# Performance work log

Measured on AMD Instinct MI355X. Metric: run time of the kernel, lower is better.

Reference implementation:

```python
import jax, jax.numpy as jnp
import numpy as np

MAX_LAB = 64  # cap on connected-component ids per sample (original cc3d is unbounded)
BIG = jnp.int32(2 ** 30)


def _cc_label(mask):
    """26-connectivity connected components of a 3D bool mask via label propagation.
    Each component ends with label == max initial voxel id in it (nonzero), bg = 0."""
    n = mask.size
    init = jnp.where(mask, jnp.arange(1, n + 1, dtype=jnp.int32).reshape(mask.shape), jnp.int32(0))

    def cond(st):
        return jnp.any(st[0] != st[1])

    def body(st):
        lab = st[0]
        # max over 3x3x3 neighborhood == 26-connectivity propagation step
        neigh = jax.lax.reduce_window(lab, jnp.int32(0), jax.lax.max, (3, 3, 3), (1, 1, 1), 'SAME')
        return (jnp.where(mask, neigh, jnp.int32(0)), lab)

    lab, _ = jax.lax.while_loop(cond, body, (init, jnp.full_like(init, -1)))
    return lab


def _compact(lab):
    """Relabel a per-sample label map to consecutive ids 0,1..k (0 = background),
    matching cc3d's 1..k numbering."""
    u = jnp.unique(lab, size=MAX_LAB + 1, fill_value=BIG)  # sorted: [0, l1, .., lk, BIG..]
    return jnp.searchsorted(u, lab).astype(jnp.int32)


def _instance_dice(x, y):
    xb = jnp.squeeze(x, 1) > 0.5  # [B,D,H,W] pred foreground
    yb = jnp.squeeze(y, 1) > 0.5  # [B,D,H,W] gt foreground
    label = jax.vmap(lambda m: _compact(_cc_label(m)))
    gt_lab = label(yb)  # per-sample ids 0..k_i (ids shared across batch, as in original)
    pr_lab = label(xb)
    M = MAX_LAB + 1
    # joint histogram over (gt component id, pred component id), global across batch
    idx = gt_lab.reshape(-1) * M + pr_lab.reshape(-1)
    overlap = jax.ops.segment_sum(jnp.ones(idx.shape, jnp.float32), idx, num_segments=M * M).reshape(M, M)
    gt_size = overlap.sum(1)  # [M] voxels per gt id
    pr_size = overlap.sum(0)  # [M] voxels per pred id
    ov = overlap[1:, 1:]                       # [G,P] fg-fg overlaps
    inter_mask = ov > 0                        # pred comp p intersects gt comp g
    inter = ov.sum(1)                          # [G] |gt_g  ∩  union(intersecting preds)|
    union_sz = (inter_mask * pr_size[1:]).sum(1)  # [G] |union of intersecting pred comps|
    has_inter = inter > 0
    dice = jnp.where(has_inter, 2.0 * inter / jnp.maximum(union_sz + gt_size[1:], 1.0), 0.0)
    lesion_dice = dice.sum()
    num_gt = jnp.sum(gt_size[1:] > 0).astype(jnp.float32)
    tp_mask = inter_mask.any(0)                # [P] pred comps matched to some gt
    num_fp = jnp.sum((pr_size[1:] > 0) & ~tp_mask).astype(jnp.float32)
    return lesion_dice / (num_gt + num_fp)


def setup_inputs() -> dict:
    B, D, H, W = 2, 128, 128, 128
    R, N_BLOBS = 5, 12
    rng = np.random.default_rng(0)
    zz, yy, xx = np.meshgrid(np.arange(D), np.arange(H), np.arange(W), indexing='ij')

    def blobs(k):
        m = np.zeros((B, D, H, W), bool)
        for b in range(B):
            c = rng.integers(R + 2, D - R - 2, size=(k, 3))
            for cz, cy, cx in c:
                m[b] |= (zz - cz) ** 2 + (yy - cy) ** 2 + (xx - cx) ** 2 <= R * R
        return m

    y = blobs(N_BLOBS)
    # prediction = slightly shifted gt (partial-overlap TPs) + extra false-positive blobs
    x = np.roll(y, shift=(2, 1, 0), axis=(1, 2, 3)) | blobs(4)
    return {"x": jnp.asarray(x[:, None].astype(np.float32)),
            "y": jnp.asarray(y[:, None].astype(np.float32))}


def reference(x, y):
    return _instance_dice(x, y)
```

## Files before the change

### kernel.cpp

```cpp
#include <hip/hip_runtime.h>


#define NVOX (128 * 128 * 128)
#define NTOT (2 * NVOX)
#define NBLK 4096
#define CAP 12288
#define ML 65
#define NSLAB 8
#define ZSLAB 16

__global__ __launch_bounds__(256) void k_count(
    const float4* __restrict__ x, const float4* __restrict__ y,
    unsigned char* __restrict__ maskArr, int* __restrict__ blkCnt) {
    int t = blockIdx.x * 256 + threadIdx.x;
    float4 xv = x[t];
    float4 yv = y[t];
    unsigned m = 0;
    if (xv.x > 0.5f) m |= 1u;
    if (xv.y > 0.5f) m |= 2u;
    if (xv.z > 0.5f) m |= 4u;
    if (xv.w > 0.5f) m |= 8u;
    if (yv.x > 0.5f) m |= 16u;
    if (yv.y > 0.5f) m |= 32u;
    if (yv.z > 0.5f) m |= 64u;
    if (yv.w > 0.5f) m |= 128u;
    maskArr[t] = (unsigned char)m;
    int pk = __popc(m & 0xFu) | (__popc(m >> 4) << 16);
    __shared__ int red[256];
    red[threadIdx.x] = pk;
    __syncthreads();
    for (int s = 128; s > 0; s >>= 1) {
        if ((int)threadIdx.x < s) red[threadIdx.x] += red[threadIdx.x + s];
        __syncthreads();
    }
    if (threadIdx.x == 0) {
        blkCnt[blockIdx.x]        = red[0] & 0xFFFF;
        blkCnt[NBLK + blockIdx.x] = red[0] >> 16;
    }
}

__global__ __launch_bounds__(1024) void k_scan(
    const int* __restrict__ blkCnt, int* __restrict__ blkOff, int* __restrict__ cnt) {
    __shared__ int buf[2][1024];
    __shared__ int segbase;
    int t = threadIdx.x;
    for (int f = 0; f < 2; ++f) {
        const int* c = blkCnt + f * NBLK;
        int* o = blkOff + f * NBLK;
        int base = t * 4;
        int a0 = c[base], a1 = c[base + 1], a2 = c[base + 2], a3 = c[base + 3];
        int s = a0 + a1 + a2 + a3;
        int src = 0;
        buf[0][t] = s;
        __syncthreads();
        for (int d = 1; d < 1024; d <<= 1) {
            int nv = buf[src][t];
            if (t >= d) nv += buf[src][t - d];
            buf[src ^ 1][t] = nv;
            src ^= 1;
            __syncthreads();
        }
        int incl = buf[src][t];
        int excl = incl - s;
        if (t == 511) segbase = incl;
        __syncthreads();
        int sub = (base >= 2048) ? segbase : 0;
        o[base]     = excl - sub;
        o[base + 1] = excl + a0 - sub;
        o[base + 2] = excl + a0 + a1 - sub;
        o[base + 3] = excl + a0 + a1 + a2 - sub;
        if (t == 511)  cnt[f * 2 + 0] = incl;
        if (t == 1023) cnt[f * 2 + 1] = incl - segbase;
        __syncthreads();
    }
}

__global__ __launch_bounds__(256) void k_fill(
    const unsigned char* __restrict__ maskArr, const int* __restrict__ blkOff,
    unsigned short* __restrict__ posMapX, unsigned short* __restrict__ posMapY,
    int* __restrict__ lists) {
    int blk = blockIdx.x;
    int t = blk * 256 + threadIdx.x;
    int b = blk >> 11;
    unsigned m = maskArr[t];
    int px = __popc(m & 0xFu), py = __popc(m >> 4);
    __shared__ int buf[2][256];
    int pk = px | (py << 16);
    int src = 0;
    buf[0][threadIdx.x] = pk;
    __syncthreads();
    for (int d = 1; d < 256; d <<= 1) {
        int nv = buf[src][threadIdx.x];
        if ((int)threadIdx.x >= d) nv += buf[src][threadIdx.x - d];
        buf[src ^ 1][threadIdx.x] = nv;
        src ^= 1;
        __syncthreads();
    }
    int incl = buf[src][threadIdx.x];
    int baseX = blkOff[blk]        + (incl & 0xFFFF) - px;
    int baseY = blkOff[NBLK + blk] + (incl >> 16)    - py;
    int i = t << 2;
    int j = i & (NVOX - 1);
    ushort4 pxv, pyv;
    unsigned short* ppx = &pxv.x;
    unsigned short* ppy = &pyv.x;
    int cx = 0, cy = 0;
    #pragma unroll
    for (int k = 0; k < 4; ++k) {
        unsigned short vx = 0, vy = 0;
        if (m & (1u << k)) {
            int pos = baseX + cx++;
            if (pos < CAP) { lists[(0 + b) * CAP + pos] = j + k; vx = (unsigned short)(pos + 1); }
        }
        if (m & (1u << (k + 4))) {
            int pos = baseY + cy++;
            if (pos < CAP) { lists[(2 + b) * CAP + pos] = j + k; vy = (unsigned short)(pos + 1); }
        }
        ppx[k] = vx;
        ppy[k] = vy;
    }
    ((ushort4*)posMapX)[t] = pxv;
    ((ushort4*)posMapY)[t] = pyv;
}

__device__ __forceinline__ int find_root(volatile unsigned* parent, int i) {
    unsigned p = parent[i];
    while (p != (unsigned)i) {
        unsigned gp = parent[p];
        if (gp != p) parent[i] = gp;
        i = (int)p;
        p = gp;
    }
    return i;
}

__device__ __forceinline__ void lds_union(unsigned* parentNV, int a, int b) {
    volatile unsigned* parent = (volatile unsigned*)parentNV;
    int ra = find_root(parent, a);
    int rb = find_root(parent, b);
    while (ra != rb) {
        int lo = ra < rb ? ra : rb;
        int hi = ra < rb ? rb : ra;
        unsigned old = atomicCAS(&parentNV[lo], (unsigned)lo, (unsigned)hi);
        if (old == (unsigned)lo) return;
        ra = find_root(parent, (int)old);
        rb = find_root(parent, hi);
    }
}

__global__ __launch_bounds__(1024) void k_cc_local(
    const unsigned short* __restrict__ posMapX, const unsigned short* __restrict__ posMapY,
    const int* __restrict__ lists, const int* __restrict__ blkOff,
    const int* __restrict__ cnt, int* __restrict__ rootPos) {
    int fb = blockIdx.y;
    int slab = blockIdx.x;
    int f = fb >> 1, b = fb & 1;
    const unsigned short* posMap = (f ? posMapY : posMapX) + (b << 21);
    const int* fgl = lists + fb * CAP;
    int n = cnt[fb]; if (n > CAP) n = CAP;
    int blkbase = b * 2048 + slab * 256;
    int s0 = blkOff[f * NBLK + blkbase];
    int s1 = (slab == NSLAB - 1) ? n : blkOff[f * NBLK + blkbase + 256];
    if (s1 > n) s1 = n;
    int ns = s1 - s0;
    if (ns <= 0) return;

    __shared__ unsigned parent[CAP];
    int tid = threadIdx.x;

    for (int q = tid; q < ns; q += 1024) {
        int p = s0 + q;
        int j = fgl[p];
        unsigned par = (unsigned)q;
        if (p + 1 < s1 && (j & 127) != 127) {
            if (fgl[p + 1] == j + 1) par = (unsigned)(q + 1);
        }
        parent[q] = par;
    }
    __syncthreads();

    for (int q = tid; q < ns; q += 1024) {
        int j = fgl[s0 + q];
        int z = j >> 14, y = (j >> 7) & 127, x0 = j & 127;
        bool ztop = ((z & (ZSLAB - 1)) == (ZSLAB - 1));
        unsigned short qv[12];
        int idx = 0;
        #pragma unroll
        for (int dx = -1; dx <= 1; ++dx) {
            int yy = y + 1, xx = x0 + dx;
            bool ok = yy <= 127 && (unsigned)xx <= 127u;
            int nj = (z << 14) + (yy << 7) + xx;
            qv[idx++] = ok ? posMap[nj] : (unsigned short)0;
        }
        #pragma unroll
        for (int dy = -1; dy <= 1; ++dy)
            #pragma unroll
            for (int dx = -1; dx <= 1; ++dx) {
                int zz = z + 1, yy = y + dy, xx = x0 + dx;
                bool ok = !ztop && zz <= 127 && (unsigned)yy <= 127u && (unsigned)xx <= 127u;
                int nj = (zz << 14) + (yy << 7) + xx;
                qv[idx++] = ok ? posMap[nj] : (unsigned short)0;
            }
        #pragma unroll
        for (int k = 0; k < 12; ++k)
            if (qv[k]) lds_union(parent, q, (int)qv[k] - 1 - s0);
    }
    __syncthreads();

    for (int q = tid; q < ns; q += 1024)
        rootPos[fb * CAP + s0 + q] = s0 + find_root((volatile unsigned*)parent, q);
}

__global__ __launch_bounds__(1024) void k_cc_merge(
    const unsigned short* __restrict__ posMapX, const unsigned short* __restrict__ posMapY,
    const int* __restrict__ lists, const int* __restrict__ cnt,
    const int* __restrict__ rootPos, unsigned char* __restrict__ compact) {
    int fb = blockIdx.x;
    int f = fb >> 1, b = fb & 1;
    const unsigned short* posMap = (f ? posMapY : posMapX) + (b << 21);
    const int* fgl = lists + fb * CAP;
    unsigned char* cmp = compact + fb * CAP;
    int tid = threadIdx.x;
    int n = cnt[fb]; if (n > CAP) n = CAP;

    __shared__ unsigned parent[CAP];
    __shared__ int rootsL[128];
    __shared__ int sortedL[64];
    __shared__ int nrSh;

    for (int p = tid; p < n; p += 1024) parent[p] = (unsigned)rootPos[fb * CAP + p];
    if (tid == 0) nrSh = 0;
    __syncthreads();

    for (int p = tid; p < n; p += 1024) {
        int j = fgl[p];
        int z = j >> 14;
        if ((z & (ZSLAB - 1)) != (ZSLAB - 1) || z == 127) continue;
        int y = (j >> 7) & 127, x0 = j & 127;
        int zz = z + 1;
        unsigned short qv[9];
        int idx = 0;
        #pragma unroll
        for (int dy = -1; dy <= 1; ++dy)
            #pragma unroll
            for (int dx = -1; dx <= 1; ++dx) {
                int yy = y + dy, xx = x0 + dx;
                bool ok = (unsigned)yy <= 127u && (unsigned)xx <= 127u;
                int nj = (zz << 14) + (yy << 7) + xx;
                qv[idx++] = ok ? posMap[nj] : (unsigned short)0;
            }
        #pragma unroll
        for (int k = 0; k < 9; ++k)
            if (qv[k]) lds_union(parent, p, (int)qv[k] - 1);
    }
    __syncthreads();

    for (int p = tid; p < n; p += 1024) {
        if (parent[p] == (unsigned)p) {
            int slot = atomicAdd(&nrSh, 1);
            if (slot < 128) rootsL[slot] = p;
        }
    }
    __syncthreads();
    int nr = nrSh; if (nr > 64) nr = 64;
    if (tid < nr) {
        int v = rootsL[tid];
        int r = 0;
        for (int k = 0; k < nr; ++k) r += (rootsL[k] < v) ? 1 : 0;
        sortedL[r] = v;
    }
    __syncthreads();

    for (int p = tid; p < n; p += 1024) {
        int r = find_root((volatile unsigned*)parent, p);
        int lo = 0, hi = nr;
        while (lo < hi) { int mid = (lo + hi) >> 1; if (sortedL[mid] < r) lo = mid + 1; else hi = mid; }
        cmp[p] = (unsigned char)(lo + 1);
    }
}

__global__ __launch_bounds__(256) void k_overlap(
    const unsigned short* __restrict__ posMapX, const unsigned short* __restrict__ posMapY,
    const int* __restrict__ lists, const int* __restrict__ cnt,
    const unsigned char* __restrict__ compact, int* __restrict__ overlap) {
    int fb = blockIdx.y;
    int f = fb >> 1, b = fb & 1;
    int n = cnt[fb]; if (n > CAP) n = CAP;
    int t = blockIdx.x * blockDim.x + threadIdx.x;
    if (t >= n) return;
    int j = lists[fb * CAP + t];
    int gi = (b << 21) + j;
    int key;
    if (f == 0) {
        int pc = (int)compact[fb * CAP + t];
        int q = (int)posMapY[gi];
        int gc = q ? (int)compact[(2 + b) * CAP + (q - 1)] : 0;
        key = gc * ML + pc;
    } else {
        if (posMapX[gi] != 0) return;
        int gc = (int)compact[fb * CAP + t];
        key = gc * ML;
    }
    unsigned long long remaining = __ballot(1);
    int lane = threadIdx.x & 63;
    while (remaining) {
        int leader = __ffsll(remaining) - 1;
        int lkey = __shfl(key, leader);
        unsigned long long m = __ballot(lkey == key ? 1 : 0) & remaining;
        if (lane == leader) atomicAdd(&overlap[lkey], (int)__popcll(m));
        remaining &= ~m;
    }
}

__global__ void k_final(const int* __restrict__ overlap, float* __restrict__ out) {
    __shared__ int O[ML * ML];
    __shared__ float prs[ML];
    __shared__ unsigned char tp[ML];
    __shared__ float diceSh[ML];
    __shared__ int ngSh[ML];
    __shared__ int nfSh[ML];
    int tid = threadIdx.x;
    for (int i = tid; i < ML * ML; i += blockDim.x) O[i] = overlap[i];
    __syncthreads();
    if (tid < ML) {
        int s = 0; int any = 0;
        for (int g = 0; g < ML; ++g) {
            int o = O[g * ML + tid];
            s += o;
            if (g >= 1 && o > 0) any = 1;
        }
        prs[tid] = (float)s;
        tp[tid] = (unsigned char)any;
    }
    __syncthreads();
    if (tid < ML) {
        float dice = 0.f; int ng = 0, nf = 0;
        if (tid >= 1) {
            int gt = 0, inter = 0; float un = 0.f;
            for (int p = 0; p < ML; ++p) {
                int o = O[tid * ML + p];
                gt += o;
                if (p >= 1) { inter += o; if (o > 0) un += prs[p]; }
            }
            if (inter > 0) {
                float den = un + (float)gt;
                if (den < 1.f) den = 1.f;
                dice = 2.f * (float)inter / den;
            }
            ng = (gt > 0) ? 1 : 0;
            nf = (prs[tid] > 0.f && tp[tid] == 0) ? 1 : 0;
        }
        diceSh[tid] = dice; ngSh[tid] = ng; nfSh[tid] = nf;
    }
    __syncthreads();
    if (tid == 0) {
        float ld = 0.f; int ng = 0, nf = 0;
        for (int k = 1; k < ML; ++k) { ld += diceSh[k]; ng += ngSh[k]; nf += nfSh[k]; }
        out[0] = ld / (float)(ng + nf);
    }
}

extern "C" void kernel_launch(void* const* d_in, const int* in_sizes, int n_in,
                              void* d_out, int out_size, void* d_ws, size_t ws_size,
                              hipStream_t stream) {
    const float* x = (const float*)d_in[0];
    const float* y = (const float*)d_in[1];
    float* out = (float*)d_out;

    char* base = (char*)d_ws;
    int* cnt            = (int*)base;
    int* overlap        = cnt + 16;
    int* blkCnt         = overlap + ML * ML;
    int* blkOff         = blkCnt + 2 * NBLK;
    int* lists          = blkOff + 2 * NBLK;
    int* rootPos        = lists + 4 * CAP;
    unsigned char* comp = (unsigned char*)(rootPos + 4 * CAP);
    unsigned char* maskArr = comp + 4 * CAP;
    size_t off = (size_t)((maskArr + NTOT / 4) - (unsigned char*)base);
    off = (off + 15) & ~(size_t)15;
    unsigned short* posMapX = (unsigned short*)(base + off);
    unsigned short* posMapY = posMapX + NTOT;

    hipMemsetAsync(overlap, 0, ML * ML * sizeof(int), stream);

    k_count<<<NBLK, 256, 0, stream>>>((const float4*)x, (const float4*)y, maskArr, blkCnt);
    k_scan<<<1, 1024, 0, stream>>>(blkCnt, blkOff, cnt);
    k_fill<<<NBLK, 256, 0, stream>>>(maskArr, blkOff, posMapX, posMapY, lists);
    k_cc_local<<<dim3(NSLAB, 4), 1024, 0, stream>>>(posMapX, posMapY, lists, blkOff, cnt, rootPos);
    k_cc_merge<<<4, 1024, 0, stream>>>(posMapX, posMapY, lists, cnt, rootPos, comp);
    k_overlap<<<dim3((CAP + 255) / 256, 4), 256, 0, stream>>>(
        posMapX, posMapY, lists, cnt, comp, overlap);
    k_final<<<1, 256, 0, stream>>>(overlap, out);
}
```

Measured before the change: 162.8 us.

## Fuse overlap histogram into CC merge, pack X/Y counts, use wave-shuffle scans

Folds the overlap histogram pass into the merge kernel, which now handles both masks of one sample per block and builds the histogram in LDS before flushing it. This removes the compact-label buffer, one kernel launch and the memset, which now happens inside k_count. The block counts for X and Y are packed into one int, so a single scan covers both, and the LDS tree reductions and scans are replaced with wave shuffles. In exchange the merge runs on only 2 blocks instead of 4, so there is less parallelism, and the LDS footprint grows because both parent arrays are held at once.

```diff
diff --git a/kernel.cpp b/kernel.cpp
--- a/kernel.cpp
+++ b/kernel.cpp
@@ -11,7 +11,8 @@
 
 __global__ __launch_bounds__(256) void k_count(
     const float4* __restrict__ x, const float4* __restrict__ y,
-    unsigned char* __restrict__ maskArr, int* __restrict__ blkCnt) {
+    unsigned char* __restrict__ maskArr, int* __restrict__ blkCnt,
+    int* __restrict__ overlap) {
     int t = blockIdx.x * 256 + threadIdx.x;
     float4 xv = x[t];
     float4 yv = y[t];
@@ -25,53 +26,50 @@
     if (yv.z > 0.5f) m |= 64u;
     if (yv.w > 0.5f) m |= 128u;
     maskArr[t] = (unsigned char)m;
-    int pk = __popc(m & 0xFu) | (__popc(m >> 4) << 16);
-    __shared__ int red[256];
-    red[threadIdx.x] = pk;
-    __syncthreads();
-    for (int s = 128; s > 0; s >>= 1) {
-        if ((int)threadIdx.x < s) red[threadIdx.x] += red[threadIdx.x + s];
-        __syncthreads();
-    }
-    if (threadIdx.x == 0) {
-        blkCnt[blockIdx.x]        = red[0] & 0xFFFF;
-        blkCnt[NBLK + blockIdx.x] = red[0] >> 16;
-    }
+    int v = __popc(m & 0xFu) | (__popc(m >> 4) << 16);
+    #pragma unroll
+    for (int d = 1; d < 64; d <<= 1) v += __shfl_xor(v, d);
+    __shared__ int ws[4];
+    if ((threadIdx.x & 63) == 0) ws[threadIdx.x >> 6] = v;
+    __syncthreads();
+    if (threadIdx.x == 0) blkCnt[blockIdx.x] = ws[0] + ws[1] + ws[2] + ws[3];
+    if (blockIdx.x == 0)
+        for (int i = threadIdx.x; i < ML * ML; i += 256) overlap[i] = 0;
 }
 
 __global__ __launch_bounds__(1024) void k_scan(
     const int* __restrict__ blkCnt, int* __restrict__ blkOff, int* __restrict__ cnt) {
-    __shared__ int buf[2][1024];
-    __shared__ int segbase;
     int t = threadIdx.x;
-    for (int f = 0; f < 2; ++f) {
-        const int* c = blkCnt + f * NBLK;
-        int* o = blkOff + f * NBLK;
-        int base = t * 4;
-        int a0 = c[base], a1 = c[base + 1], a2 = c[base + 2], a3 = c[base + 3];
-        int s = a0 + a1 + a2 + a3;
-        int src = 0;
-        buf[0][t] = s;
-        __syncthreads();
-        for (int d = 1; d < 1024; d <<= 1) {
-            int nv = buf[src][t];
-            if (t >= d) nv += buf[src][t - d];
-            buf[src ^ 1][t] = nv;
-            src ^= 1;
-            __syncthreads();
-        }
-        int incl = buf[src][t];
-        int excl = incl - s;
-        if (t == 511) segbase = incl;
-        __syncthreads();
-        int sub = (base >= 2048) ? segbase : 0;
-        o[base]     = excl - sub;
-        o[base + 1] = excl + a0 - sub;
-        o[base + 2] = excl + a0 + a1 - sub;
-        o[base + 3] = excl + a0 + a1 + a2 - sub;
-        if (t == 511)  cnt[f * 2 + 0] = incl;
-        if (t == 1023) cnt[f * 2 + 1] = incl - segbase;
-        __syncthreads();
+    int base = t * 4;
+    int a0 = blkCnt[base], a1 = blkCnt[base + 1], a2 = blkCnt[base + 2], a3 = blkCnt[base + 3];
+    int s = a0 + a1 + a2 + a3;
+    int lane = t & 63, wave = t >> 6;
+    int v = s;
+    #pragma unroll
+    for (int d = 1; d < 64; d <<= 1) {
+        int u = __shfl_up(v, d);
+        if (lane >= d) v += u;
+    }
+    __shared__ int wsum[16];
+    __shared__ int segb;
+    if (lane == 63) wsum[wave] = v;
+    __syncthreads();
+    int woff = 0;
+    for (int k = 0; k < wave; ++k) woff += wsum[k];
+    int incl = v + woff;
+    int excl = incl - s;
+    if (t == 511) segb = incl;
+    __syncthreads();
+    int sub = (base >= 2048) ? segb : 0;
+    int e0 = excl - sub;
+    blkOff[base]     = e0;
+    blkOff[base + 1] = e0 + a0;
+    blkOff[base + 2] = e0 + a0 + a1;
+    blkOff[base + 3] = e0 + a0 + a1 + a2;
+    if (t == 511) { cnt[0] = incl & 0xFFFF; cnt[2] = incl >> 16; }
+    if (t == 1023) {
+        cnt[1] = (incl & 0xFFFF) - (segb & 0xFFFF);
+        cnt[3] = (incl >> 16)    - (segb >> 16);
     }
 }
 
@@ -84,21 +82,23 @@
     int b = blk >> 11;
     unsigned m = maskArr[t];
     int px = __popc(m & 0xFu), py = __popc(m >> 4);
-    __shared__ int buf[2][256];
     int pk = px | (py << 16);
-    int src = 0;
-    buf[0][threadIdx.x] = pk;
-    __syncthreads();
-    for (int d = 1; d < 256; d <<= 1) {
-        int nv = buf[src][threadIdx.x];
-        if ((int)threadIdx.x >= d) nv += buf[src][threadIdx.x - d];
-        buf[src ^ 1][threadIdx.x] = nv;
-        src ^= 1;
-        __syncthreads();
-    }
-    int incl = buf[src][threadIdx.x];
-    int baseX = blkOff[blk]        + (incl & 0xFFFF) - px;
-    int baseY = blkOff[NBLK + blk] + (incl >> 16)    - py;
+    int lane = threadIdx.x & 63, wave = threadIdx.x >> 6;
+    int v = pk;
+    #pragma unroll
+    for (int d = 1; d < 64; d <<= 1) {
+        int u = __shfl_up(v, d);
+        if (lane >= d) v += u;
+    }
+    __shared__ int wsum[4];
+    if (lane == 63) wsum[wave] = v;
+    __syncthreads();
+    int woff = 0;
+    for (int k = 0; k < wave; ++k) woff += wsum[k];
+    int incl = v + woff;
+    int off = blkOff[blk];
+    int baseX = (off & 0xFFFF) + (incl & 0xFFFF) - px;
+    int baseY = (off >> 16)    + (incl >> 16)    - py;
     int i = t << 2;
     int j = i & (NVOX - 1);
     ushort4 pxv, pyv;
@@ -159,8 +159,11 @@
     const int* fgl = lists + fb * CAP;
     int n = cnt[fb]; if (n > CAP) n = CAP;
     int blkbase = b * 2048 + slab * 256;
-    int s0 = blkOff[f * NBLK + blkbase];
-    int s1 = (slab == NSLAB - 1) ? n : blkOff[f * NBLK + blkbase + 256];
+    int o0 = blkOff[blkbase];
+    int s0 = f ? (o0 >> 16) : (o0 & 0xFFFF);
+    int s1;
+    if (slab == NSLAB - 1) s1 = n;
+    else { int o1 = blkOff[blkbase + 256]; s1 = f ? (o1 >> 16) : (o1 & 0xFFFF); }
     if (s1 > n) s1 = n;
     int ns = s1 - s0;
     if (ns <= 0) return;
@@ -211,104 +214,122 @@
         rootPos[fb * CAP + s0 + q] = s0 + find_root((volatile unsigned*)parent, q);
 }
 
-__global__ __launch_bounds__(1024) void k_cc_merge(
-    const unsigned short* __restrict__ posMapX, const unsigned short* __restrict__ posMapY,
-    const int* __restrict__ lists, const int* __restrict__ cnt,
-    const int* __restrict__ rootPos, unsigned char* __restrict__ compact) {
-    int fb = blockIdx.x;
-    int f = fb >> 1, b = fb & 1;
-    const unsigned short* posMap = (f ? posMapY : posMapX) + (b << 21);
-    const int* fgl = lists + fb * CAP;
-    unsigned char* cmp = compact + fb * CAP;
-    int tid = threadIdx.x;
-    int n = cnt[fb]; if (n > CAP) n = CAP;
-
-    __shared__ unsigned parent[CAP];
-    __shared__ int rootsL[128];
-    __shared__ int sortedL[64];
-    __shared__ int nrSh;
-
-    for (int p = tid; p < n; p += 1024) parent[p] = (unsigned)rootPos[fb * CAP + p];
-    if (tid == 0) nrSh = 0;
-    __syncthreads();
-
-    for (int p = tid; p < n; p += 1024) {
-        int j = fgl[p];
-        int z = j >> 14;
-        if ((z & (ZSLAB - 1)) != (ZSLAB - 1) || z == 127) continue;
-        int y = (j >> 7) & 127, x0 = j & 127;
-        int zz = z + 1;
-        unsigned short qv[9];
-        int idx = 0;
-        #pragma unroll
-        for (int dy = -1; dy <= 1; ++dy)
-            #pragma unroll
-            for (int dx = -1; dx <= 1; ++dx) {
-                int yy = y + dy, xx = x0 + dx;
-                bool ok = (unsigned)yy <= 127u && (unsigned)xx <= 127u;
-                int nj = (zz << 14) + (yy << 7) + xx;
-                qv[idx++] = ok ? posMap[nj] : (unsigned short)0;
-            }
-        #pragma unroll
-        for (int k = 0; k < 9; ++k)
-            if (qv[k]) lds_union(parent, p, (int)qv[k] - 1);
-    }
-    __syncthreads();
-
-    for (int p = tid; p < n; p += 1024) {
-        if (parent[p] == (unsigned)p) {
-            int slot = atomicAdd(&nrSh, 1);
-            if (slot < 128) rootsL[slot] = p;
-        }
-    }
-    __syncthreads();
-    int nr = nrSh; if (nr > 64) nr = 64;
-    if (tid < nr) {
-        int v = rootsL[tid];
-        int r = 0;
-        for (int k = 0; k < nr; ++k) r += (rootsL[k] < v) ? 1 : 0;
-        sortedL[r] = v;
-    }
-    __syncthreads();
-
-    for (int p = tid; p < n; p += 1024) {
-        int r = find_root((volatile unsigned*)parent, p);
-        int lo = 0, hi = nr;
-        while (lo < hi) { int mid = (lo + hi) >> 1; if (sortedL[mid] < r) lo = mid + 1; else hi = mid; }
-        cmp[p] = (unsigned char)(lo + 1);
-    }
-}
-
-__global__ __launch_bounds__(256) void k_overlap(
-    const unsigned short* __restrict__ posMapX, const unsigned short* __restrict__ posMapY,
-    const int* __restrict__ lists, const int* __restrict__ cnt,
-    const unsigned char* __restrict__ compact, int* __restrict__ overlap) {
-    int fb = blockIdx.y;
-    int f = fb >> 1, b = fb & 1;
-    int n = cnt[fb]; if (n > CAP) n = CAP;
-    int t = blockIdx.x * blockDim.x + threadIdx.x;
-    if (t >= n) return;
-    int j = lists[fb * CAP + t];
-    int gi = (b << 21) + j;
-    int key;
-    if (f == 0) {
-        int pc = (int)compact[fb * CAP + t];
-        int q = (int)posMapY[gi];
-        int gc = q ? (int)compact[(2 + b) * CAP + (q - 1)] : 0;
-        key = gc * ML + pc;
-    } else {
-        if (posMapX[gi] != 0) return;
-        int gc = (int)compact[fb * CAP + t];
-        key = gc * ML;
-    }
+__device__ __forceinline__ int rank_of(const int* sortedL, int nr, int v) {
+    int lo = 0, hi = nr;
+    while (lo < hi) { int mid = (lo + hi) >> 1; if (sortedL[mid] < v) lo = mid + 1; else hi = mid; }
+    return lo;
+}
+
+__device__ __forceinline__ void hist_add(int* ovl, int key) {
     unsigned long long remaining = __ballot(1);
     int lane = threadIdx.x & 63;
     while (remaining) {
         int leader = __ffsll(remaining) - 1;
         int lkey = __shfl(key, leader);
         unsigned long long m = __ballot(lkey == key ? 1 : 0) & remaining;
-        if (lane == leader) atomicAdd(&overlap[lkey], (int)__popcll(m));
+        if (lane == leader) atomicAdd(&ovl[lkey], (int)__popcll(m));
         remaining &= ~m;
+    }
+}
+
+__global__ __launch_bounds__(1024) void k_cc_merge(
+    const unsigned short* __restrict__ posMapX, const unsigned short* __restrict__ posMapY,
+    const int* __restrict__ lists, const int* __restrict__ cnt,
+    const int* __restrict__ rootPos, int* __restrict__ overlap) {
+    int b = blockIdx.x;
+    int tid = threadIdx.x;
+    int nX = cnt[b];     if (nX > CAP) nX = CAP;
+    int nY = cnt[2 + b]; if (nY > CAP) nY = CAP;
+
+    __shared__ unsigned par[2][CAP];
+    __shared__ int sortedL[2][64];
+    __shared__ int rootsL[128];
+    __shared__ int nrA[2];
+    __shared__ int ovl[ML * ML];
+
+    for (int p = tid; p < nX; p += 1024) par[0][p] = (unsigned)rootPos[b * CAP + p];
+    for (int p = tid; p < nY; p += 1024) par[1][p] = (unsigned)rootPos[(2 + b) * CAP + p];
+    for (int i = tid; i < ML * ML; i += 1024) ovl[i] = 0;
+    if (tid < 2) nrA[tid] = 0;
+    __syncthreads();
+
+    for (int f = 0; f < 2; ++f) {
+        const unsigned short* pm = (f ? posMapY : posMapX) + (b << 21);
+        const int* fgl = lists + (f * 2 + b) * CAP;
+        int n = f ? nY : nX;
+        unsigned* P = par[f];
+        for (int p = tid; p < n; p += 1024) {
+            int j = fgl[p];
+            int z = j >> 14;
+            if ((z & (ZSLAB - 1)) != (ZSLAB - 1) || z == 127) continue;
+            int y = (j >> 7) & 127, x0 = j & 127;
+            int zz = z + 1;
+            unsigned short qv[9];
+            int idx = 0;
+            #pragma unroll
+            for (int dy = -1; dy <= 1; ++dy)
+                #pragma unroll
+                for (int dx = -1; dx <= 1; ++dx) {
+                    int yy = y + dy, xx = x0 + dx;
+                    bool ok = (unsigned)yy <= 127u && (unsigned)xx <= 127u;
+                    int nj = (zz << 14) + (yy << 7) + xx;
+                    qv[idx++] = ok ? pm[nj] : (unsigned short)0;
+                }
+            #pragma unroll
+            for (int k = 0; k < 9; ++k)
+                if (qv[k]) lds_union(P, p, (int)qv[k] - 1);
+        }
+    }
+    __syncthreads();
+
+    for (int f = 0; f < 2; ++f) {
+        int n = f ? nY : nX;
+        unsigned* P = par[f];
+        for (int p = tid; p < n; p += 1024)
+            if (P[p] == (unsigned)p) {
+                int s = atomicAdd(&nrA[f], 1);
+                if (s < 128) rootsL[s] = p;
+            }
+        __syncthreads();
+        int nr = nrA[f]; if (nr > 64) nr = 64;
+        if (tid < nr) {
+            int v = rootsL[tid];
+            int r = 0;
+            for (int k = 0; k < nr; ++k) r += (rootsL[k] < v) ? 1 : 0;
+            sortedL[f][r] = v;
+        }
+        __syncthreads();
+    }
+    int nr0 = nrA[0]; if (nr0 > 64) nr0 = 64;
+    int nr1 = nrA[1]; if (nr1 > 64) nr1 = 64;
+
+    {
+        const int* fglX = lists + (0 + b) * CAP;
+        for (int t = tid; t < nX; t += 1024) {
+            int j = fglX[t];
+            int rX = find_root((volatile unsigned*)par[0], t);
+            int pc = 1 + rank_of(sortedL[0], nr0, rX);
+            int q = (int)posMapY[(b << 21) + j];
+            int gc = 0;
+            if (q) {
+                int rY = find_root((volatile unsigned*)par[1], q - 1);
+                gc = 1 + rank_of(sortedL[1], nr1, rY);
+            }
+            hist_add(ovl, gc * ML + pc);
+        }
+        const int* fglY = lists + (2 + b) * CAP;
+        for (int t = tid; t < nY; t += 1024) {
+            int j = fglY[t];
+            if (posMapX[(b << 21) + j]) continue;
+            int rY = find_root((volatile unsigned*)par[1], t);
+            int gc = 1 + rank_of(sortedL[1], nr1, rY);
+            hist_add(ovl, gc * ML);
+        }
+    }
+    __syncthreads();
+    for (int i = tid; i < ML * ML; i += 1024) {
+        int v = ovl[i];
+        if (v) atomicAdd(&overlap[i], v);
     }
 }
 
@@ -371,24 +392,20 @@
     int* cnt            = (int*)base;
     int* overlap        = cnt + 16;
     int* blkCnt         = overlap + ML * ML;
-    int* blkOff         = blkCnt + 2 * NBLK;
-    int* lists          = blkOff + 2 * NBLK;
+    int* blkOff         = blkCnt + NBLK;
+    int* lists          = blkOff + NBLK;
     int* rootPos        = lists + 4 * CAP;
-    unsigned char* comp = (unsigned char*)(rootPos + 4 * CAP);
-    unsigned char* maskArr = comp + 4 * CAP;
+    unsigned char* maskArr = (unsigned char*)(rootPos + 4 * CAP);
     size_t off = (size_t)((maskArr + NTOT / 4) - (unsigned char*)base);
     off = (off + 15) & ~(size_t)15;
     unsigned short* posMapX = (unsigned short*)(base + off);
     unsigned short* posMapY = posMapX + NTOT;
 
-    hipMemsetAsync(overlap, 0, ML * ML * sizeof(int), stream);
-
-    k_count<<<NBLK, 256, 0, stream>>>((const float4*)x, (const float4*)y, maskArr, blkCnt);
+    k_count<<<NBLK, 256, 0, stream>>>((const float4*)x, (const float4*)y,
+                                      maskArr, blkCnt, overlap);
     k_scan<<<1, 1024, 0, stream>>>(blkCnt, blkOff, cnt);
     k_fill<<<NBLK, 256, 0, stream>>>(maskArr, blkOff, posMapX, posMapY, lists);
     k_cc_local<<<dim3(NSLAB, 4), 1024, 0, stream>>>(posMapX, posMapY, lists, blkOff, cnt, rootPos);
-    k_cc_merge<<<4, 1024, 0, stream>>>(posMapX, posMapY, lists, cnt, rootPos, comp);
-    k_overlap<<<dim3((CAP + 255) / 256, 4), 256, 0, stream>>>(
-        posMapX, posMapY, lists, cnt, comp, overlap);
+    k_cc_merge<<<2, 1024, 0, stream>>>(posMapX, posMapY, lists, cnt, rootPos, overlap);
     k_final<<<1, 256, 0, stream>>>(overlap, out);
 }
```

Measured after the change: 172.5 us. 1.06x slower.
